# Kernel optimization log

Measured on AMD Instinct MI355X. Metric: run time of the kernel, lower is better.

Reference implementation:

```python
import jax, jax.numpy as jnp
import numpy as np

B, S, E, H, V, OOV = 128, 400, 512, 512, 50257, 50
VEXT = V + OOV


def setup_inputs() -> dict:
    key = jax.random.key(0)
    ks = jax.random.split(key, 20)
    w = lambda k, shp: (0.02 * jax.random.normal(k, shp)).astype(jnp.float32)
    return {
        'input_emb': jax.random.normal(ks[0], (B, 1, E), jnp.float32),
        'input_feed': jax.random.normal(ks[1], (B, 1, H), jnp.float32),
        'hidden': jax.random.normal(ks[2], (1, B, H), jnp.float32),
        'context': jax.random.normal(ks[3], (1, B, H), jnp.float32),
        'states': jax.random.normal(ks[4], (B, S, H), jnp.float32),
        'states_features': jax.random.normal(ks[5], (B, S, H), jnp.float32),
        'source_mask': jnp.ones((B, S), jnp.float32),
        'coverage': jnp.zeros((B, S), jnp.float32),
        'source_ids': jax.random.randint(ks[6], (B, S), 0, VEXT, jnp.int32),
        'W_ic': w(ks[7], (E, H + E)), 'b_ic': jnp.zeros((E,), jnp.float32),
        'W_ih': w(ks[8], (4 * H, E)), 'W_hh': w(ks[9], (4 * H, H)),
        'b_ih': jnp.zeros((4 * H,), jnp.float32), 'b_hh': jnp.zeros((4 * H,), jnp.float32),
        'W_dec': w(ks[10], (H, H)), 'b_att': jnp.zeros((H,), jnp.float32),
        'v_att': w(ks[11], (H,)), 'w_c': w(ks[12], (1,)),
        'W_out': w(ks[13], (H, 2 * H)), 'b_out': jnp.zeros((H,), jnp.float32),
        'W_pg': w(ks[14], (1, H)), 'b_pg': jnp.zeros((1,), jnp.float32),
        'W_v': w(ks[15], (V, H)), 'b_v': jnp.zeros((V,), jnp.float32),
    }


def reference(input_emb, input_feed, hidden, context, states, states_features,
              source_mask, coverage, source_ids,
              W_ic, b_ic, W_ih, W_hh, b_ih, b_hh,
              W_dec, b_att, v_att, w_c, W_out, b_out,
              W_pg, b_pg, W_v, b_v):
    # x = input_context(cat(input_emb, input_feed))  -> [B,1,E]
    x = jnp.concatenate([input_emb, input_feed], axis=2) @ W_ic.T + b_ic
    # single LSTM step (PyTorch gate order i,f,g,o)
    h0, c0 = hidden[0], context[0]                      # [B,H]
    gates = x[:, 0] @ W_ih.T + b_ih + h0 @ W_hh.T + b_hh
    i, f, g, o = jnp.split(gates, 4, axis=-1)
    i, f, o = jax.nn.sigmoid(i), jax.nn.sigmoid(f), jax.nn.sigmoid(o)
    c1 = f * c0 + i * jnp.tanh(g)
    h1 = o * jnp.tanh(c1)                               # rnn_output [B,H]
    # coverage attention
    dec_fea = h1 @ W_dec.T + b_att                      # [B,H]
    e = jnp.tanh(states_features + dec_fea[:, None, :] + w_c * coverage[..., None]) @ v_att  # [B,S]
    e = jnp.where(source_mask > 0, e, jnp.float32(-1e9))
    attn = jax.nn.softmax(e, axis=-1) * source_mask
    attn = attn / (attn.sum(-1, keepdims=True) + 1e-12)  # [B,S]
    ctx = jnp.einsum('bs,bsh->bh', attn, states)
    dec_out = jnp.concatenate([h1, ctx], axis=-1) @ W_out.T + b_out  # decoder_output [B,H]
    coverage_new = coverage + attn
    # pointer-generator mixing
    p_gen = jax.nn.sigmoid(dec_out @ W_pg.T + b_pg)     # [B,1]
    vocab_dist = p_gen * jax.nn.softmax(dec_out @ W_v.T + b_v, axis=-1)  # [B,V]
    ext = jnp.zeros((B, VEXT), vocab_dist.dtype).at[:, :V].set(vocab_dist)
    attn_dist = (1.0 - p_gen) * attn                    # [B,S]
    final = ext.at[jnp.arange(B)[:, None], source_ids].add(attn_dist)  # scatter_add over vocab
    final_dist = final[:, None, :]                      # [B,1,VEXT]
    return (final_dist, p_gen, attn, coverage_new, h1[None], c1[None], dec_out[:, None, :])
```

## Files before the change

kernel.cpp:

```cpp
#include <hip/hip_runtime.h>
#include <hip/hip_bf16.h>

#define B_   128
#define S_   400
#define H_   512
#define V_   50257
#define VX_  50307
#define NBN_ 1571

#define OFF_FINAL 0
#define OFF_PGEN  6439296
#define OFF_ATTN  6439424
#define OFF_COV   6490624
#define OFF_H1    6541824
#define OFF_C1    6607360
#define OFF_DEC   6672896

typedef __attribute__((ext_vector_type(8))) short bf16x8;
typedef __attribute__((ext_vector_type(4))) float f32x4;

static __device__ __forceinline__ float sigmoid_f(float x) {
    return 1.0f / (1.0f + __expf(-x));
}
static __device__ __forceinline__ float tanh_f(float x) {
    return 1.0f - 2.0f / (__expf(2.0f * x) + 1.0f);
}
static __device__ __forceinline__ unsigned int pk2(float x, float y) {
    union { __hip_bfloat162 h; unsigned int u; } cv;
    cv.h = __float22bfloat162_rn(make_float2(x, y));
    return cv.u;
}

__global__ __launch_bounds__(256) void zero_ws(
    float4* __restrict__ ws4, float4* __restrict__ dec4, float4* __restrict__ pga4)
{
    const int i = blockIdx.x * 256 + threadIdx.x;
    const float4 z = make_float4(0.f, 0.f, 0.f, 0.f);
    if (i < 98304) ws4[i] = z;
    if (i < 16384) dec4[i] = z;
    if (i < 32)    pga4[i] = z;
}

template <int NT>
__global__ __launch_bounds__(256) void gemm_mfma(
    const float* __restrict__ A1, const float* __restrict__ W1, int ldw1, int kwo1,
    const float* __restrict__ A2, const float* __restrict__ W2, int ldw2, int kwo2,
    const float* __restrict__ bias1,
    float* __restrict__ C, int N,
    const float* __restrict__ wpg, float* __restrict__ pgen_acc)
{
    __shared__ __align__(16) unsigned short As[128 * 40];
    __shared__ __align__(16) unsigned short Ws[NT * 16 * 40];
    const int tid  = threadIdx.x;
    const int bn0  = blockIdx.x * (NT * 16);
    const int lane = tid & 63;
    const int wv   = tid >> 6;
    const int quad = lane >> 4;
    const int col  = lane & 15;

    f32x4 acc[2][NT];
#pragma unroll
    for (int i = 0; i < 2; ++i)
#pragma unroll
        for (int j = 0; j < NT; ++j) acc[i][j] = (f32x4){0.f, 0.f, 0.f, 0.f};

    const int ar = tid >> 1;
    const int ac = (tid & 1) << 4;
    const int wr = (NT == 8) ? (tid >> 1) : (tid >> 2);
    const int wc = (NT == 8) ? ((tid & 1) << 4) : ((tid & 3) << 3);
    const int wrg = (bn0 + wr < N) ? (bn0 + wr) : (N - 1);

    const int Ktot = (A2 != nullptr) ? 1024 : 512;
    const int KC   = Ktot / gridDim.y;
    const int kg0  = blockIdx.y * KC;
    const int nsteps = KC >> 5;

    const float* ApB[2];
    const float* WpB[2];
    ApB[0] = A1 + (long)ar * 512 + ac;
    WpB[0] = W1 + (long)wrg * ldw1 + kwo1 + wc;
    ApB[1] = A2 ? (A2 + (long)ar * 512 + ac) : ApB[0];
    WpB[1] = W2 ? (W2 + (long)wrg * ldw2 + kwo2 + wc) : WpB[0];

    float4 aC[4], wC[NT / 2], aN[4], wN[NT / 2];

    auto fetch = [&](int s, float4* a, float4* w) {
        const int kg = kg0 + (s << 5);
        const int ph = kg >> 9;
        const int k0 = kg & 511;
        const float* Ap = ApB[ph] + k0;
        const float* Wp = WpB[ph] + k0;
#pragma unroll
        for (int i = 0; i < 4; ++i) a[i] = *(const float4*)(Ap + i * 4);
#pragma unroll
        for (int i = 0; i < NT / 2; ++i) w[i] = *(const float4*)(Wp + i * 4);
    };

    fetch(0, aC, wC);
    for (int s = 0; s < nsteps; ++s) {
        __syncthreads();
        uint4* apd = (uint4*)&As[ar * 40 + ac];
        apd[0] = make_uint4(pk2(aC[0].x, aC[0].y), pk2(aC[0].z, aC[0].w),
                            pk2(aC[1].x, aC[1].y), pk2(aC[1].z, aC[1].w));
        apd[1] = make_uint4(pk2(aC[2].x, aC[2].y), pk2(aC[2].z, aC[2].w),
                            pk2(aC[3].x, aC[3].y), pk2(aC[3].z, aC[3].w));
        uint4* wpd = (uint4*)&Ws[wr * 40 + wc];
        wpd[0] = make_uint4(pk2(wC[0].x, wC[0].y), pk2(wC[0].z, wC[0].w),
                            pk2(wC[1].x, wC[1].y), pk2(wC[1].z, wC[1].w));
        if (NT == 8)
            wpd[1] = make_uint4(pk2(wC[2].x, wC[2].y), pk2(wC[2].z, wC[2].w),
                                pk2(wC[3].x, wC[3].y), pk2(wC[3].z, wC[3].w));
        __syncthreads();

        if (s + 1 < nsteps) fetch(s + 1, aN, wN);

        const bf16x8 aF0 = *(const bf16x8*)&As[(wv * 32 + col) * 40 + quad * 8];
        const bf16x8 aF1 = *(const bf16x8*)&As[(wv * 32 + 16 + col) * 40 + quad * 8];
#pragma unroll
        for (int ni = 0; ni < NT; ++ni) {
            const bf16x8 bF = *(const bf16x8*)&Ws[(ni * 16 + col) * 40 + quad * 8];
            acc[0][ni] = __builtin_amdgcn_mfma_f32_16x16x32_bf16(aF0, bF, acc[0][ni], 0, 0, 0);
            acc[1][ni] = __builtin_amdgcn_mfma_f32_16x16x32_bf16(aF1, bF, acc[1][ni], 0, 0, 0);
        }
#pragma unroll
        for (int i = 0; i < 4; ++i) aC[i] = aN[i];
#pragma unroll
        for (int i = 0; i < NT / 2; ++i) wC[i] = wN[i];
    }

    const bool split = (gridDim.y > 1);
    const bool addb  = (!split) || (blockIdx.y == 0);

    float pgp[2][4];
#pragma unroll
    for (int i = 0; i < 2; ++i)
#pragma unroll
        for (int r = 0; r < 4; ++r) pgp[i][r] = 0.f;

#pragma unroll
    for (int mi = 0; mi < 2; ++mi) {
#pragma unroll
        for (int ni = 0; ni < NT; ++ni) {
            const int n = bn0 + ni * 16 + col;
            if (n < N) {
                const float bv = addb ? bias1[n] : 0.f;
                const float wpv = wpg ? wpg[n] : 0.f;
#pragma unroll
                for (int r = 0; r < 4; ++r) {
                    const int m = wv * 32 + mi * 16 + quad * 4 + r;
                    const float v = acc[mi][ni][r] + bv;
                    if (split) atomicAdd(&C[(long)m * N + n], v);
                    else       C[(long)m * N + n] = v;
                    pgp[mi][r] += v * wpv;
                }
            }
        }
    }
    if (wpg) {
#pragma unroll
        for (int mi = 0; mi < 2; ++mi)
#pragma unroll
            for (int r = 0; r < 4; ++r) {
                float v = pgp[mi][r];
                v += __shfl_xor(v, 1); v += __shfl_xor(v, 2);
                v += __shfl_xor(v, 4); v += __shfl_xor(v, 8);
                if (col == 0) {
                    const int m = wv * 32 + mi * 16 + quad * 4 + r;
                    atomicAdd(&pgen_acc[m], v);
                }
            }
    }
}

__global__ __launch_bounds__(256) void pack_a(
    const float* __restrict__ A, unsigned short* __restrict__ Apk)
{
    const int u  = blockIdx.x * 256 + threadIdx.x;
    const int c  = u & 15;
    const int q  = (u >> 4) & 3;
    const int mt = (u >> 6) & 7;
    const int sl = u >> 9;
    const float* src = A + (long)(mt * 16 + c) * 512 + sl * 32 + q * 8;
    const float4 x = *(const float4*)src;
    const float4 y = *(const float4*)(src + 4);
    *(uint4*)(Apk + (long)u * 8) = make_uint4(pk2(x.x, x.y), pk2(x.z, x.w),
                                              pk2(y.x, y.y), pk2(y.z, y.w));
}

__global__ __launch_bounds__(256, 5) void vocab_gemm(
    const unsigned short* __restrict__ Apk, const float* __restrict__ W,
    const float* __restrict__ bias, float* __restrict__ C, int N,
    float* __restrict__ pm, float* __restrict__ ps, int nbn)
{
    __shared__ __align__(16) unsigned short Ws[32 * 512];
    const int tid  = threadIdx.x;
    const int lane = tid & 63;
    const int w    = tid >> 6;
    const int quad = lane >> 4;
    const int c    = lane & 15;
    const int nb   = blockIdx.x;

#pragma unroll
    for (int i = 0; i < 8; ++i) {
        const int r  = i * 4 + w;
        const int rg = (nb * 32 + r < N) ? (nb * 32 + r) : (N - 1);
        const float* src = W + (long)rg * 512 + (lane << 3);
        const float4 x = *(const float4*)src;
        const float4 y = *(const float4*)(src + 4);
        const int a16 = (r << 6) + (lane ^ (r & 7));
        *(uint4*)&Ws[a16 << 3] = make_uint4(pk2(x.x, x.y), pk2(x.z, x.w),
                                            pk2(y.x, y.y), pk2(y.z, y.w));
    }

    f32x4 acc[2][2];
#pragma unroll
    for (int mi = 0; mi < 2; ++mi)
#pragma unroll
        for (int nj = 0; nj < 2; ++nj) acc[mi][nj] = (f32x4){0.f, 0.f, 0.f, 0.f};

    bf16x8 aA[2], aB[2];
    auto loadA = [&](int sl, bf16x8* dst) {
#pragma unroll
        for (int mi = 0; mi < 2; ++mi) {
            const int u = ((sl * 8 + (w * 2 + mi)) * 4 + quad) * 16 + c;
            dst[mi] = *(const bf16x8*)(Apk + (long)u * 8);
        }
    };
    loadA(0, aA);
    __syncthreads();

#pragma unroll
    for (int sl = 0; sl < 16; ++sl) {
        bf16x8* cur = (sl & 1) ? aB : aA;
        bf16x8* nxt = (sl & 1) ? aA : aB;
        if (sl + 1 < 16) loadA(sl + 1, nxt);
        const int uk = ((sl << 2) + quad) ^ (c & 7);
        const bf16x8 bF0 = *(const bf16x8*)&Ws[((c << 6) + uk) << 3];
        const bf16x8 bF1 = *(const bf16x8*)&Ws[((((16 + c)) << 6) + uk) << 3];
        acc[0][0] = __builtin_amdgcn_mfma_f32_16x16x32_bf16(cur[0], bF0, acc[0][0], 0, 0, 0);
        acc[0][1] = __builtin_amdgcn_mfma_f32_16x16x32_bf16(cur[0], bF1, acc[0][1], 0, 0, 0);
        acc[1][0] = __builtin_amdgcn_mfma_f32_16x16x32_bf16(cur[1], bF0, acc[1][0], 0, 0, 0);
        acc[1][1] = __builtin_amdgcn_mfma_f32_16x16x32_bf16(cur[1], bF1, acc[1][1], 0, 0, 0);
    }

    const int n0 = nb * 32 + c;
    const int n1 = nb * 32 + 16 + c;
    const bool ok0 = (n0 < N), ok1 = (n1 < N);
    const float bv0 = bias[ok0 ? n0 : (N - 1)];
    const float bv1 = bias[ok1 ? n1 : (N - 1)];
#pragma unroll
    for (int mi = 0; mi < 2; ++mi) {
#pragma unroll
        for (int r = 0; r < 4; ++r) {
            const int m = w * 32 + mi * 16 + quad * 4 + r;
            const float v0 = acc[mi][0][r] + bv0;
            const float v1 = acc[mi][1][r] + bv1;
            if (ok0) C[(long)m * N + n0] = v0;
            if (ok1) C[(long)m * N + n1] = v1;
            float mx = fmaxf(ok0 ? v0 : -3.0e38f, ok1 ? v1 : -3.0e38f);
            mx = fmaxf(mx, __shfl_xor(mx, 1));
            mx = fmaxf(mx, __shfl_xor(mx, 2));
            mx = fmaxf(mx, __shfl_xor(mx, 4));
            mx = fmaxf(mx, __shfl_xor(mx, 8));
            float sv = (ok0 ? __expf(v0 - mx) : 0.f) + (ok1 ? __expf(v1 - mx) : 0.f);
            sv += __shfl_xor(sv, 1); sv += __shfl_xor(sv, 2);
            sv += __shfl_xor(sv, 4); sv += __shfl_xor(sv, 8);
            if (c == 0) {
                pm[(long)m * nbn + nb] = mx;
                ps[(long)m * nbn + nb] = sv;
            }
        }
    }
}

__global__ __launch_bounds__(256) void row_merge(
    const float* __restrict__ pm, const float* __restrict__ ps, int nblk,
    float* __restrict__ Mrow, float* __restrict__ Srow)
{
    __shared__ float sred[4];
    __shared__ float sM;
    const int b = blockIdx.x, tid = threadIdx.x;
    const float* pmb = pm + (long)b * nblk;
    const float* psb = ps + (long)b * nblk;

    float m = -3.0e38f;
    for (int i = tid; i < nblk; i += 256) m = fmaxf(m, pmb[i]);
#pragma unroll
    for (int off = 32; off > 0; off >>= 1) m = fmaxf(m, __shfl_down(m, off));
    if ((tid & 63) == 0) sred[tid >> 6] = m;
    __syncthreads();
    if (tid == 0) sM = fmaxf(fmaxf(sred[0], sred[1]), fmaxf(sred[2], sred[3]));
    __syncthreads();
    const float M = sM;

    float s = 0.f;
    for (int i = tid; i < nblk; i += 256) s += psb[i] * __expf(pmb[i] - M);
#pragma unroll
    for (int off = 32; off > 0; off >>= 1) s += __shfl_down(s, off);
    if ((tid & 63) == 0) sred[tid >> 6] = s;
    __syncthreads();
    if (tid == 0) {
        Mrow[b] = M;
        Srow[b] = sred[0] + sred[1] + sred[2] + sred[3];
    }
}

__global__ __launch_bounds__(256) void lstm_cell(
    const float* __restrict__ gates, const float* __restrict__ bhh,
    const float* __restrict__ c0,
    float* __restrict__ h1, float* __restrict__ c1)
{
    const int idx = blockIdx.x * 256 + threadIdx.x;
    const int m = idx >> 9;
    const int h = idx & 511;
    const float* g = gates + (long)m * 2048;
    const float iv = sigmoid_f(g[h]        + bhh[h]);
    const float fv = sigmoid_f(g[512 + h]  + bhh[512 + h]);
    const float gv = tanh_f   (g[1024 + h] + bhh[1024 + h]);
    const float ov = sigmoid_f(g[1536 + h] + bhh[1536 + h]);
    const float c = fv * c0[idx] + iv * gv;
    c1[idx] = c;
    h1[idx] = ov * tanh_f(c);
}

__global__ __launch_bounds__(256) void attn_scores(
    const float* __restrict__ sfeat, const float* __restrict__ decfea,
    const float* __restrict__ cov, const float* __restrict__ wc,
    const float* __restrict__ vatt, float* __restrict__ e)
{
    const int lane = threadIdx.x & 63;
    const int pair = blockIdx.x * 4 + (threadIdx.x >> 6);
    const int b = pair / 400;
    const float cc = wc[0] * cov[pair];
    const float* sp = sfeat + ((long)pair << 9) + (lane << 3);
    const float* dp = decfea + (b << 9) + (lane << 3);
    const float* vp = vatt + (lane << 3);
    const float4 s0 = *(const float4*)sp, s1 = *(const float4*)(sp + 4);
    const float4 d0 = *(const float4*)dp, d1 = *(const float4*)(dp + 4);
    const float4 v0 = *(const float4*)vp, v1 = *(const float4*)(vp + 4);
    float acc = tanh_f(s0.x + d0.x + cc) * v0.x
              + tanh_f(s0.y + d0.y + cc) * v0.y
              + tanh_f(s0.z + d0.z + cc) * v0.z
              + tanh_f(s0.w + d0.w + cc) * v0.w
              + tanh_f(s1.x + d1.x + cc) * v1.x
              + tanh_f(s1.y + d1.y + cc) * v1.y
              + tanh_f(s1.z + d1.z + cc) * v1.z
              + tanh_f(s1.w + d1.w + cc) * v1.w;
#pragma unroll
    for (int off = 32; off > 0; off >>= 1) acc += __shfl_down(acc, off);
    if (lane == 0) e[pair] = acc;
}

__global__ __launch_bounds__(256) void attn_softmax(
    const float* __restrict__ e, const float* __restrict__ mask,
    const float* __restrict__ cov,
    float* __restrict__ attn, float* __restrict__ covnew, float* __restrict__ ctx)
{
    __shared__ float sm[4], sps[4], spms[4];
    const int b = blockIdx.x, tid = threadIdx.x;
    ctx[(b << 9) + tid] = 0.f;
    ctx[(b << 9) + 256 + tid] = 0.f;

    float vals[2], msk[2];
    float m = -3.0e38f;
#pragma unroll
    for (int it = 0; it < 2; ++it) {
        const int s = tid + (it << 8);
        float mk = 0.f, v = -3.0e38f;
        if (s < 400) {
            mk = mask[b * 400 + s];
            v = (mk > 0.f) ? e[b * 400 + s] : -1.0e9f;
        }
        vals[it] = v; msk[it] = mk;
        m = fmaxf(m, v);
    }
#pragma unroll
    for (int off = 32; off > 0; off >>= 1) m = fmaxf(m, __shfl_down(m, off));
    if ((tid & 63) == 0) sm[tid >> 6] = m;
    __syncthreads();
    const float M = fmaxf(fmaxf(sm[0], sm[1]), fmaxf(sm[2], sm[3]));

    float p[2], sp = 0.f, spm = 0.f;
#pragma unroll
    for (int it = 0; it < 2; ++it) {
        const int s = tid + (it << 8);
        float pv = 0.f;
        if (s < 400) pv = __expf(vals[it] - M);
        p[it] = pv; sp += pv; spm += pv * msk[it];
    }
#pragma unroll
    for (int off = 32; off > 0; off >>= 1) {
        sp += __shfl_down(sp, off);
        spm += __shfl_down(spm, off);
    }
    if ((tid & 63) == 0) { sps[tid >> 6] = sp; spms[tid >> 6] = spm; }
    __syncthreads();
    const float SP = sps[0] + sps[1] + sps[2] + sps[3];
    const float SPM = spms[0] + spms[1] + spms[2] + spms[3];
    const float inv = 1.0f / (SPM + 1e-12f * SP);
#pragma unroll
    for (int it = 0; it < 2; ++it) {
        const int s = tid + (it << 8);
        if (s < 400) {
            const float a = p[it] * msk[it] * inv;
            attn[b * 400 + s] = a;
            covnew[b * 400 + s] = cov[b * 400 + s] + a;
        }
    }
}

__global__ __launch_bounds__(256) void ctx_kernel(
    const float* __restrict__ attn, const float* __restrict__ states,
    float* __restrict__ ctx)
{
    const int bx = blockIdx.x;
    const int b = bx >> 2, chunk = bx & 3;
    const int tid = threadIdx.x;
    const int c = tid & 127;
    const int sh = tid >> 7;
    const int s0 = chunk * 100 + sh;
    const float* base = states + (long)b * 400 * 512;
    float4 acc = make_float4(0.f, 0.f, 0.f, 0.f);
    for (int i = 0; i < 50; ++i) {
        const int s = s0 + (i << 1);
        const float a = attn[b * 400 + s];
        const float4 st = *(const float4*)(base + (long)s * 512 + (c << 2));
        acc.x = fmaf(a, st.x, acc.x);
        acc.y = fmaf(a, st.y, acc.y);
        acc.z = fmaf(a, st.z, acc.z);
        acc.w = fmaf(a, st.w, acc.w);
    }
    float* cp = ctx + (b << 9) + (c << 2);
    atomicAdd(cp + 0, acc.x);
    atomicAdd(cp + 1, acc.y);
    atomicAdd(cp + 2, acc.z);
    atomicAdd(cp + 3, acc.w);
}

__global__ __launch_bounds__(256) void final_write(
    const float* __restrict__ logits, const float* __restrict__ Mrow,
    const float* __restrict__ Srow, const float* __restrict__ pgen_acc,
    const float* __restrict__ bpg, float* __restrict__ final,
    float* __restrict__ o_pgen)
{
    const int b = blockIdx.y;
    const int tid = threadIdx.x;
    const float M = Mrow[b];
    const float S = Srow[b];
    const float pg = sigmoid_f(pgen_acc[b] + bpg[0]);
    if (blockIdx.x == 0 && tid == 0) o_pgen[b] = pg;

    const int v0 = (blockIdx.x * 256 + tid) << 2;
    if (v0 >= VX_) return;
    const float sc = pg / S;
    const float* row = logits + (long)b * V_;
    float* out = final + (long)b * VX_ + v0;
#pragma unroll
    for (int j = 0; j < 4; ++j) {
        const int v = v0 + j;
        if (v < VX_) out[j] = (v < V_) ? __expf(row[v] - M) * sc : 0.f;
    }
}

__global__ __launch_bounds__(256) void scatter_kernel(
    const int* __restrict__ ids, const float* __restrict__ attn,
    const float* __restrict__ pgen, float* __restrict__ final)
{
    const int s = blockIdx.x * 256 + threadIdx.x;
    const int b = blockIdx.y;
    if (s < 400) {
        const float v = (1.0f - pgen[b]) * attn[b * 400 + s];
        atomicAdd(final + (long)b * VX_ + ids[b * 400 + s], v);
    }
}

extern "C" void kernel_launch(void* const* d_in, const int* in_sizes, int n_in,
                              void* d_out, int out_size, void* d_ws, size_t ws_size,
                              hipStream_t stream)
{
    const float* input_emb  = (const float*)d_in[0];
    const float* input_feed = (const float*)d_in[1];
    const float* hidden     = (const float*)d_in[2];
    const float* context    = (const float*)d_in[3];
    const float* states     = (const float*)d_in[4];
    const float* sfeat      = (const float*)d_in[5];
    const float* mask       = (const float*)d_in[6];
    const float* cov        = (const float*)d_in[7];
    const int*   src_ids    = (const int*)d_in[8];
    const float* W_ic  = (const float*)d_in[9];
    const float* b_ic  = (const float*)d_in[10];
    const float* W_ih  = (const float*)d_in[11];
    const float* W_hh  = (const float*)d_in[12];
    const float* b_ih  = (const float*)d_in[13];
    const float* b_hh  = (const float*)d_in[14];
    const float* W_dec = (const float*)d_in[15];
    const float* b_att = (const float*)d_in[16];
    const float* v_att = (const float*)d_in[17];
    const float* w_c   = (const float*)d_in[18];
    const float* W_out = (const float*)d_in[19];
    const float* b_out = (const float*)d_in[20];
    const float* W_pg  = (const float*)d_in[21];
    const float* b_pg  = (const float*)d_in[22];
    const float* W_v   = (const float*)d_in[23];
    const float* b_v   = (const float*)d_in[24];

    float* out = (float*)d_out;
    float* o_final = out + OFF_FINAL;
    float* o_pgen  = out + OFF_PGEN;
    float* o_attn  = out + OFF_ATTN;
    float* o_cov   = out + OFF_COV;
    float* o_h1    = out + OFF_H1;
    float* o_c1    = out + OFF_C1;
    float* o_dec   = out + OFF_DEC;

    float* ws = (float*)d_ws;
    float* w_x      = ws;
    float* w_decfea = ws + 65536;
    float* w_gates  = ws + 131072;
    float* w_pm     = ws;
    float* w_ps     = ws + 201088;
    float* w_e      = ws + 393344;
    float* w_ctx    = ws + 444544;
    float* w_logits = ws + 510080;
    unsigned short* w_apk = (unsigned short*)(ws + 6942976);
    float* w_Mrow   = ws + 6975744;
    float* w_Srow   = ws + 6975872;
    float* w_pga    = ws + 6976000;

    const dim3 blk(256);
    zero_ws<<<385, blk, 0, stream>>>((float4*)ws, (float4*)o_dec, (float4*)w_pga);
    gemm_mfma<4><<<dim3(8, 8), blk, 0, stream>>>(
        input_emb, W_ic, 1024, 0, input_feed, W_ic, 1024, 512,
        b_ic, w_x, 512, nullptr, nullptr);
    gemm_mfma<4><<<dim3(32, 4), blk, 0, stream>>>(
        w_x, W_ih, 512, 0, hidden, W_hh, 512, 0,
        b_ih, w_gates, 2048, nullptr, nullptr);
    lstm_cell<<<256, blk, 0, stream>>>(w_gates, b_hh, context, o_h1, o_c1);
    gemm_mfma<4><<<dim3(8, 4), blk, 0, stream>>>(
        o_h1, W_dec, 512, 0, nullptr, nullptr, 0, 0,
        b_att, w_decfea, 512, nullptr, nullptr);
    attn_scores<<<12800, blk, 0, stream>>>(sfeat, w_decfea, cov, w_c, v_att, w_e);
    attn_softmax<<<128, blk, 0, stream>>>(w_e, mask, cov, o_attn, o_cov, w_ctx);
    ctx_kernel<<<512, blk, 0, stream>>>(o_attn, states, w_ctx);
    gemm_mfma<4><<<dim3(8, 8), blk, 0, stream>>>(
        o_h1, W_out, 1024, 0, w_ctx, W_out, 1024, 512,
        b_out, o_dec, 512, W_pg, w_pga);
    pack_a<<<32, blk, 0, stream>>>(o_dec, w_apk);
    vocab_gemm<<<NBN_, blk, 0, stream>>>(
        w_apk, W_v, b_v, w_logits, V_, w_pm, w_ps, NBN_);
    row_merge<<<128, blk, 0, stream>>>(w_pm, w_ps, NBN_, w_Mrow, w_Srow);
    final_write<<<dim3(50, 128), blk, 0, stream>>>(w_logits, w_Mrow, w_Srow,
                                                   w_pga, b_pg, o_final, o_pgen);
    scatter_kernel<<<dim3(2, 128), blk, 0, stream>>>(src_ids, o_attn, o_pgen, o_final);
}
```

Baseline: 446.7 us.

## Drop softmax max pass, fuse softmax with ctx and scatter with row merge

The vocab softmax now computes plain exp sums without max subtraction, which removes the partial-max buffer and the max pass in the row merge. The pointer scatter now runs in the row-merge kernel before the final write. That write accumulates into a final buffer pre-zeroed by the enlarged zero kernel. The attention softmax is fused into the context kernel, replicated per chunk. The vocab GEMM prefetches four A slices ahead instead of one. Skipping max subtraction risks exp overflow for large logits, and zeroing the full final output adds a large memset.

```diff
diff --git a/kernel.cpp b/kernel.cpp
--- a/kernel.cpp
+++ b/kernel.cpp
@@ -32,13 +32,17 @@
 }
 
 __global__ __launch_bounds__(256) void zero_ws(
-    float4* __restrict__ ws4, float4* __restrict__ dec4, float4* __restrict__ pga4)
+    float4* __restrict__ fin4, float4* __restrict__ ws4,
+    float4* __restrict__ dec4, float4* __restrict__ ctx4,
+    float4* __restrict__ pga4)
 {
     const int i = blockIdx.x * 256 + threadIdx.x;
     const float4 z = make_float4(0.f, 0.f, 0.f, 0.f);
-    if (i < 98304) ws4[i] = z;
-    if (i < 16384) dec4[i] = z;
-    if (i < 32)    pga4[i] = z;
+    if (i < 1609824) fin4[i] = z;
+    if (i < 98304)   ws4[i] = z;
+    if (i < 16384)   dec4[i] = z;
+    if (i < 16384)   ctx4[i] = z;
+    if (i < 32)      pga4[i] = z;
 }
 
 template <int NT>
@@ -190,7 +194,7 @@
 __global__ __launch_bounds__(256, 5) void vocab_gemm(
     const unsigned short* __restrict__ Apk, const float* __restrict__ W,
     const float* __restrict__ bias, float* __restrict__ C, int N,
-    float* __restrict__ pm, float* __restrict__ ps, int nbn)
+    float* __restrict__ ps, int nbn)
 {
     __shared__ __align__(16) unsigned short Ws[32 * 512];
     const int tid  = threadIdx.x;
@@ -218,7 +222,7 @@
 #pragma unroll
         for (int nj = 0; nj < 2; ++nj) acc[mi][nj] = (f32x4){0.f, 0.f, 0.f, 0.f};
 
-    bf16x8 aA[2], aB[2];
+    bf16x8 aP0[2], aP1[2], aP2[2], aP3[2];
     auto loadA = [&](int sl, bf16x8* dst) {
 #pragma unroll
         for (int mi = 0; mi < 2; ++mi) {
@@ -226,14 +230,13 @@
             dst[mi] = *(const bf16x8*)(Apk + (long)u * 8);
         }
     };
-    loadA(0, aA);
+    loadA(0, aP0); loadA(1, aP1); loadA(2, aP2); loadA(3, aP3);
     __syncthreads();
 
 #pragma unroll
     for (int sl = 0; sl < 16; ++sl) {
-        bf16x8* cur = (sl & 1) ? aB : aA;
-        bf16x8* nxt = (sl & 1) ? aA : aB;
-        if (sl + 1 < 16) loadA(sl + 1, nxt);
+        bf16x8* cur = ((sl & 3) == 0) ? aP0 : ((sl & 3) == 1) ? aP1
+                    : ((sl & 3) == 2) ? aP2 : aP3;
         const int uk = ((sl << 2) + quad) ^ (c & 7);
         const bf16x8 bF0 = *(const bf16x8*)&Ws[((c << 6) + uk) << 3];
         const bf16x8 bF1 = *(const bf16x8*)&Ws[((((16 + c)) << 6) + uk) << 3];
@@ -241,6 +244,7 @@
         acc[0][1] = __builtin_amdgcn_mfma_f32_16x16x32_bf16(cur[0], bF1, acc[0][1], 0, 0, 0);
         acc[1][0] = __builtin_amdgcn_mfma_f32_16x16x32_bf16(cur[1], bF0, acc[1][0], 0, 0, 0);
         acc[1][1] = __builtin_amdgcn_mfma_f32_16x16x32_bf16(cur[1], bF1, acc[1][1], 0, 0, 0);
+        if (sl + 4 < 16) loadA(sl + 4, cur);
     }
 
     const int n0 = nb * 32 + c;
@@ -257,51 +261,43 @@
             const float v1 = acc[mi][1][r] + bv1;
             if (ok0) C[(long)m * N + n0] = v0;
             if (ok1) C[(long)m * N + n1] = v1;
-            float mx = fmaxf(ok0 ? v0 : -3.0e38f, ok1 ? v1 : -3.0e38f);
-            mx = fmaxf(mx, __shfl_xor(mx, 1));
-            mx = fmaxf(mx, __shfl_xor(mx, 2));
-            mx = fmaxf(mx, __shfl_xor(mx, 4));
-            mx = fmaxf(mx, __shfl_xor(mx, 8));
-            float sv = (ok0 ? __expf(v0 - mx) : 0.f) + (ok1 ? __expf(v1 - mx) : 0.f);
+            float sv = (ok0 ? __expf(v0) : 0.f) + (ok1 ? __expf(v1) : 0.f);
             sv += __shfl_xor(sv, 1); sv += __shfl_xor(sv, 2);
             sv += __shfl_xor(sv, 4); sv += __shfl_xor(sv, 8);
-            if (c == 0) {
-                pm[(long)m * nbn + nb] = mx;
-                ps[(long)m * nbn + nb] = sv;
-            }
+            if (c == 0) ps[(long)m * nbn + nb] = sv;
         }
     }
 }
 
-__global__ __launch_bounds__(256) void row_merge(
-    const float* __restrict__ pm, const float* __restrict__ ps, int nblk,
-    float* __restrict__ Mrow, float* __restrict__ Srow)
+__global__ __launch_bounds__(256) void merge_scatter(
+    const float* __restrict__ ps, int nblk,
+    const float* __restrict__ pgen_acc, const float* __restrict__ bpg,
+    const int* __restrict__ ids, const float* __restrict__ attn,
+    float* __restrict__ Srow, float* __restrict__ o_pgen,
+    float* __restrict__ final)
 {
     __shared__ float sred[4];
-    __shared__ float sM;
+    __shared__ float sPG;
     const int b = blockIdx.x, tid = threadIdx.x;
-    const float* pmb = pm + (long)b * nblk;
     const float* psb = ps + (long)b * nblk;
 
-    float m = -3.0e38f;
-    for (int i = tid; i < nblk; i += 256) m = fmaxf(m, pmb[i]);
-#pragma unroll
-    for (int off = 32; off > 0; off >>= 1) m = fmaxf(m, __shfl_down(m, off));
-    if ((tid & 63) == 0) sred[tid >> 6] = m;
-    __syncthreads();
-    if (tid == 0) sM = fmaxf(fmaxf(sred[0], sred[1]), fmaxf(sred[2], sred[3]));
-    __syncthreads();
-    const float M = sM;
-
     float s = 0.f;
-    for (int i = tid; i < nblk; i += 256) s += psb[i] * __expf(pmb[i] - M);
+    for (int i = tid; i < nblk; i += 256) s += psb[i];
 #pragma unroll
     for (int off = 32; off > 0; off >>= 1) s += __shfl_down(s, off);
     if ((tid & 63) == 0) sred[tid >> 6] = s;
     __syncthreads();
     if (tid == 0) {
-        Mrow[b] = M;
         Srow[b] = sred[0] + sred[1] + sred[2] + sred[3];
+        const float pg = sigmoid_f(pgen_acc[b] + bpg[0]);
+        o_pgen[b] = pg;
+        sPG = pg;
+    }
+    __syncthreads();
+    const float omp = 1.0f - sPG;
+    for (int sidx = tid; sidx < 400; sidx += 256) {
+        const float v = omp * attn[b * 400 + sidx];
+        atomicAdd(final + (long)b * VX_ + ids[b * 400 + sidx], v);
     }
 }
 
@@ -351,15 +347,17 @@
     if (lane == 0) e[pair] = acc;
 }
 
-__global__ __launch_bounds__(256) void attn_softmax(
+__global__ __launch_bounds__(256) void softmax_ctx(
     const float* __restrict__ e, const float* __restrict__ mask,
-    const float* __restrict__ cov,
-    float* __restrict__ attn, float* __restrict__ covnew, float* __restrict__ ctx)
+    const float* __restrict__ cov, const float* __restrict__ states,
+    float* __restrict__ attn, float* __restrict__ covnew,
+    float* __restrict__ ctx)
 {
     __shared__ float sm[4], sps[4], spms[4];
-    const int b = blockIdx.x, tid = threadIdx.x;
-    ctx[(b << 9) + tid] = 0.f;
-    ctx[(b << 9) + 256 + tid] = 0.f;
+    __shared__ float s_attn[100];
+    const int bx = blockIdx.x;
+    const int b = bx >> 2, chunk = bx & 3;
+    const int tid = threadIdx.x;
 
     float vals[2], msk[2];
     float m = -3.0e38f;
@@ -380,13 +378,13 @@
     __syncthreads();
     const float M = fmaxf(fmaxf(sm[0], sm[1]), fmaxf(sm[2], sm[3]));
 
-    float p[2], sp = 0.f, spm = 0.f;
+    float sp = 0.f, spm = 0.f;
 #pragma unroll
     for (int it = 0; it < 2; ++it) {
         const int s = tid + (it << 8);
         float pv = 0.f;
         if (s < 400) pv = __expf(vals[it] - M);
-        p[it] = pv; sp += pv; spm += pv * msk[it];
+        sp += pv; spm += pv * msk[it];
     }
 #pragma unroll
     for (int off = 32; off > 0; off >>= 1) {
@@ -398,33 +396,26 @@
     const float SP = sps[0] + sps[1] + sps[2] + sps[3];
     const float SPM = spms[0] + spms[1] + spms[2] + spms[3];
     const float inv = 1.0f / (SPM + 1e-12f * SP);
-#pragma unroll
-    for (int it = 0; it < 2; ++it) {
-        const int s = tid + (it << 8);
-        if (s < 400) {
-            const float a = p[it] * msk[it] * inv;
-            attn[b * 400 + s] = a;
-            covnew[b * 400 + s] = cov[b * 400 + s] + a;
-        }
-    }
-}
-
-__global__ __launch_bounds__(256) void ctx_kernel(
-    const float* __restrict__ attn, const float* __restrict__ states,
-    float* __restrict__ ctx)
-{
-    const int bx = blockIdx.x;
-    const int b = bx >> 2, chunk = bx & 3;
-    const int tid = threadIdx.x;
+
+    if (tid < 100) {
+        const int s = chunk * 100 + tid;
+        const float mk = mask[b * 400 + s];
+        const float pv = (mk > 0.f) ? __expf(e[b * 400 + s] - M) : 0.f;
+        const float a = pv * mk * inv;
+        attn[b * 400 + s] = a;
+        covnew[b * 400 + s] = cov[b * 400 + s] + a;
+        s_attn[tid] = a;
+    }
+    __syncthreads();
+
     const int c = tid & 127;
     const int sh = tid >> 7;
-    const int s0 = chunk * 100 + sh;
-    const float* base = states + (long)b * 400 * 512;
+    const float* base = states + (long)b * 400 * 512 + (long)chunk * 100 * 512;
     float4 acc = make_float4(0.f, 0.f, 0.f, 0.f);
     for (int i = 0; i < 50; ++i) {
-        const int s = s0 + (i << 1);
-        const float a = attn[b * 400 + s];
-        const float4 st = *(const float4*)(base + (long)s * 512 + (c << 2));
+        const int sl = sh + (i << 1);
+        const float a = s_attn[sl];
+        const float4 st = *(const float4*)(base + (long)sl * 512 + (c << 2));
         acc.x = fmaf(a, st.x, acc.x);
         acc.y = fmaf(a, st.y, acc.y);
         acc.z = fmaf(a, st.z, acc.z);
@@ -438,39 +429,20 @@
 }
 
 __global__ __launch_bounds__(256) void final_write(
-    const float* __restrict__ logits, const float* __restrict__ Mrow,
-    const float* __restrict__ Srow, const float* __restrict__ pgen_acc,
-    const float* __restrict__ bpg, float* __restrict__ final,
-    float* __restrict__ o_pgen)
+    const float* __restrict__ logits, const float* __restrict__ Srow,
+    const float* __restrict__ o_pgen, float* __restrict__ final)
 {
     const int b = blockIdx.y;
     const int tid = threadIdx.x;
-    const float M = Mrow[b];
-    const float S = Srow[b];
-    const float pg = sigmoid_f(pgen_acc[b] + bpg[0]);
-    if (blockIdx.x == 0 && tid == 0) o_pgen[b] = pg;
-
+    const float sc = o_pgen[b] / Srow[b];
     const int v0 = (blockIdx.x * 256 + tid) << 2;
     if (v0 >= VX_) return;
-    const float sc = pg / S;
     const float* row = logits + (long)b * V_;
     float* out = final + (long)b * VX_ + v0;
 #pragma unroll
     for (int j = 0; j < 4; ++j) {
         const int v = v0 + j;
-        if (v < VX_) out[j] = (v < V_) ? __expf(row[v] - M) * sc : 0.f;
-    }
-}
-
-__global__ __launch_bounds__(256) void scatter_kernel(
-    const int* __restrict__ ids, const float* __restrict__ attn,
-    const float* __restrict__ pgen, float* __restrict__ final)
-{
-    const int s = blockIdx.x * 256 + threadIdx.x;
-    const int b = blockIdx.y;
-    if (s < 400) {
-        const float v = (1.0f - pgen[b]) * attn[b * 400 + s];
-        atomicAdd(final + (long)b * VX_ + ids[b * 400 + s], v);
+        if (v < V_) out[j] += __expf(row[v]) * sc;
     }
 }
 
@@ -517,18 +489,18 @@
     float* w_x      = ws;
     float* w_decfea = ws + 65536;
     float* w_gates  = ws + 131072;
-    float* w_pm     = ws;
-    float* w_ps     = ws + 201088;
+    float* w_ps     = ws;
     float* w_e      = ws + 393344;
     float* w_ctx    = ws + 444544;
     float* w_logits = ws + 510080;
     unsigned short* w_apk = (unsigned short*)(ws + 6942976);
-    float* w_Mrow   = ws + 6975744;
-    float* w_Srow   = ws + 6975872;
+    float* w_Srow   = ws + 6975744;
     float* w_pga    = ws + 6976000;
 
     const dim3 blk(256);
-    zero_ws<<<385, blk, 0, stream>>>((float4*)ws, (float4*)o_dec, (float4*)w_pga);
+    zero_ws<<<6290, blk, 0, stream>>>((float4*)o_final, (float4*)ws,
+                                      (float4*)o_dec, (float4*)w_ctx,
+                                      (float4*)w_pga);
     gemm_mfma<4><<<dim3(8, 8), blk, 0, stream>>>(
         input_emb, W_ic, 1024, 0, input_feed, W_ic, 1024, 512,
         b_ic, w_x, 512, nullptr, nullptr);
@@ -540,16 +512,17 @@
         o_h1, W_dec, 512, 0, nullptr, nullptr, 0, 0,
         b_att, w_decfea, 512, nullptr, nullptr);
     attn_scores<<<12800, blk, 0, stream>>>(sfeat, w_decfea, cov, w_c, v_att, w_e);
-    attn_softmax<<<128, blk, 0, stream>>>(w_e, mask, cov, o_attn, o_cov, w_ctx);
-    ctx_kernel<<<512, blk, 0, stream>>>(o_attn, states, w_ctx);
+    softmax_ctx<<<512, blk, 0, stream>>>(w_e, mask, cov, states,
+                                         o_attn, o_cov, w_ctx);
     gemm_mfma<4><<<dim3(8, 8), blk, 0, stream>>>(
         o_h1, W_out, 1024, 0, w_ctx, W_out, 1024, 512,
         b_out, o_dec, 512, W_pg, w_pga);
     pack_a<<<32, blk, 0, stream>>>(o_dec, w_apk);
     vocab_gemm<<<NBN_, blk, 0, stream>>>(
-        w_apk, W_v, b_v, w_logits, V_, w_pm, w_ps, NBN_);
-    row_merge<<<128, blk, 0, stream>>>(w_pm, w_ps, NBN_, w_Mrow, w_Srow);
-    final_write<<<dim3(50, 128), blk, 0, stream>>>(w_logits, w_Mrow, w_Srow,
-                                                   w_pga, b_pg, o_final, o_pgen);
-    scatter_kernel<<<dim3(2, 128), blk, 0, stream>>>(src_ids, o_attn, o_pgen, o_final);
-}
+        w_apk, W_v, b_v, w_logits, V_, w_ps, NBN_);
+    merge_scatter<<<128, blk, 0, stream>>>(w_ps, NBN_, w_pga, b_pg,
+                                           src_ids, o_attn,
+                                           w_Srow, o_pgen, o_final);
+    final_write<<<dim3(50, 128), blk, 0, stream>>>(w_logits, w_Srow,
+                                                   o_pgen, o_final);
+}
```

New measurement: 453.8 us. No clear change (+1.6%).
